# Kernel tuning notes

Hardware: AMD Instinct MI355X
Metric: run time of the kernel (lower is better)

## Reference

```python
import jax, jax.numpy as jnp
import numpy as np

BANDWIDTH = 1.0  # init kwarg: bandwidth; sphere mode -> var_s = gamma = bandwidth
LOG2PI = float(np.log(2.0 * np.pi))


def setup_inputs() -> dict:
    key = jax.random.key(0)
    k1, k2, k3, k4 = jax.random.split(key, 4)
    x = jax.random.normal(k1, (4096, 256), dtype=jnp.float32)
    y = jax.random.normal(k2, (4096, 128), dtype=jnp.float32)
    x_s = jax.random.normal(k3, (8192, 256), dtype=jnp.float32)
    y_s = jax.random.normal(k4, (8192, 128), dtype=jnp.float32)
    return {"x": x, "y": y, "x_s": x_s, "y_s": y_s}


def _sq_dists(a, b):
    # ||a_i - b_j||^2 via GEMM expansion: (batch, num_s)
    a2 = jnp.sum(a * a, axis=-1)[:, None]
    b2 = jnp.sum(b * b, axis=-1)[None, :]
    return a2 + b2 - 2.0 * jnp.einsum("bd,sd->bs", a, b)


def reference(x, y, x_s, y_s):
    x_dim = x.shape[-1]
    y_dim = y.shape[-1]
    var_s = BANDWIDTH
    gamma = BANDWIDTH
    logA_x = x_dim * (LOG2PI + jnp.log(jnp.float32(var_s)))
    logA_y = y_dim * (LOG2PI + jnp.log(jnp.float32(gamma)))

    sdx = _sq_dists(x, x_s) / var_s  # (batch, num_s)
    sdy = _sq_dists(y, y_s) / gamma  # (batch, num_s)

    E_log_pxy = jax.nn.logsumexp(-0.5 * (logA_x + logA_y + sdx + sdy), axis=-1)
    E_log_px = jax.nn.logsumexp(-0.5 * (logA_x + sdx), axis=-1)
    E_log_py = jax.nn.logsumexp(-0.5 * (logA_y + sdy), axis=-1)
    return jnp.mean(E_log_pxy - E_log_px - E_log_py)
```

## Files before the change

### kernel.cpp

```cpp
#include <hip/hip_runtime.h>
#include <hip/hip_bf16.h>
#include <stdint.h>

#define B_N 4096
#define S_N 8192
#define KX  256
#define KY  128
#define BM  128
#define BN  128

#define INV_LN2 1.4426950408889634f
#define LN2_F   0.6931471805599453f

typedef __bf16 bf16x8 __attribute__((ext_vector_type(8)));
typedef float  f32x4  __attribute__((ext_vector_type(4)));

__device__ __forceinline__ float exp2g(float x) { return __builtin_amdgcn_exp2f(x); }
__device__ __forceinline__ float log2g(float x) { return __builtin_amdgcn_logf(x); }

#define OFF_XH   ((size_t)0)
#define OFF_YH   ((size_t)2097152)
#define OFF_SXH  ((size_t)3145728)
#define OFF_SYH  ((size_t)7340032)
#define OFF_NX   ((size_t)9437184)
#define OFF_NY   (OFF_NX + 16384)
#define OFF_NSX  (OFF_NY + 16384)
#define OFF_NSY  (OFF_NSX + 32768)
#define OFF_PART (OFF_NSY + 32768)
#define OFF_BSUM (OFF_PART + (size_t)3*64*4096*2*4)

__device__ __forceinline__ void gl2lds16(const void* g, void* l) {
  typedef const __attribute__((address_space(1))) unsigned int* gp_t;
  typedef __attribute__((address_space(3))) unsigned int* lp_t;
  __builtin_amdgcn_global_load_lds((gp_t)g, (lp_t)l, 16, 0, 0);
}

__device__ __forceinline__ unsigned short f2bf(float f) {
  unsigned u = __builtin_bit_cast(unsigned, f);
  return (unsigned short)((u + 0x7fffu + ((u >> 16) & 1u)) >> 16);
}

__global__ __launch_bounds__(256) void conv_all(const float* __restrict__ x,
                                                const float* __restrict__ y,
                                                const float* __restrict__ xs,
                                                const float* __restrict__ ys,
                                                char* __restrict__ ws) {
  int b    = blockIdx.x;
  int wave = threadIdx.x >> 6;
  int lane = threadIdx.x & 63;
  const float* src; unsigned short* hi; float* nrm;
  int K, row; float scale;
  if (b < 1024) {
    src = x;  hi = (unsigned short*)(ws + OFF_XH);
    nrm = (float*)(ws + OFF_NX); K = 256; row = b * 4 + wave; scale = INV_LN2;
  } else if (b < 2048) {
    src = y;  hi = (unsigned short*)(ws + OFF_YH);
    nrm = (float*)(ws + OFF_NY); K = 128; row = (b - 1024) * 4 + wave; scale = INV_LN2;
  } else if (b < 4096) {
    src = xs; hi = (unsigned short*)(ws + OFF_SXH);
    nrm = (float*)(ws + OFF_NSX); K = 256; row = (b - 2048) * 4 + wave; scale = 1.0f;
  } else {
    src = ys; hi = (unsigned short*)(ws + OFF_SYH);
    nrm = (float*)(ws + OFF_NSY); K = 128; row = (b - 4096) * 4 + wave; scale = 1.0f;
  }
  float acc = 0.f;
  if (K == 256) {
    float4 v = ((const float4*)(src + (size_t)row * 256))[lane];
    float vv[4] = {v.x, v.y, v.z, v.w};
    ushort4 h4;
    unsigned short* hp = (unsigned short*)&h4;
    #pragma unroll
    for (int k = 0; k < 4; ++k) {
      acc = fmaf(vv[k], vv[k], acc);
      hp[k] = f2bf(vv[k] * scale);
    }
    ((ushort4*)(hi + (size_t)row * 256))[lane] = h4;
  } else {
    float2 v = ((const float2*)(src + (size_t)row * 128))[lane];
    float vv[2] = {v.x, v.y};
    ushort2 h2;
    unsigned short* hp = (unsigned short*)&h2;
    #pragma unroll
    for (int k = 0; k < 2; ++k) {
      acc = fmaf(vv[k], vv[k], acc);
      hp[k] = f2bf(vv[k] * scale);
    }
    ((ushort2*)(hi + (size_t)row * 128))[lane] = h2;
  }
  #pragma unroll
  for (int o = 32; o > 0; o >>= 1) acc += __shfl_down(acc, o);
  if (lane == 0) nrm[row] = acc * (-0.5f * INV_LN2);
}

__global__ __launch_bounds__(512, 4) void mie_main(const char* __restrict__ ws,
                                                   float* __restrict__ part) {
  __shared__ __align__(16) char smem[65536];

  const int tid  = threadIdx.x;
  const int lane = tid & 63;
  const int wave = tid >> 6;
  const int c    = lane & 15;
  const int q    = lane >> 4;
  const int wm   = wave >> 1;
  const int wn   = wave & 1;

  const int b     = blockIdx.x;
  const int xcd   = b & 7;
  const int w     = b >> 3;
  const int bm_t  = w & 31;
  const int sn_t  = xcd * 8 + (w >> 5);
  const int bm0   = bm_t * BM;
  const int sn0   = sn_t * BN;

  const char* xh  = ws + OFF_XH;
  const char* yh  = ws + OFF_YH;
  const char* sxh = ws + OFF_SXH;
  const char* syh = ws + OFF_SYH;
  const float* nx  = (const float*)(ws + OFF_NX);
  const float* ny  = (const float*)(ws + OFF_NY);
  const float* nsx = (const float*)(ws + OFF_NSX);
  const float* nsy = (const float*)(ws + OFF_NSY);

  auto stage = [&](int kc, char* base) {
    const char *ah, *bh; int rb, k0b;
    if (kc < 8) { ah = xh; bh = sxh; rb = 512; k0b = kc * 64; }
    else        { ah = yh; bh = syh; rb = 256; k0b = (kc - 8) * 64; }
    int l  = wave * 64 + lane;
    int r  = l >> 2;
    int sl = l & 3;
    int g  = sl ^ ((r >> 1) & 3);
    size_t kofs = (size_t)k0b + (size_t)g * 16;
    size_t goA  = (size_t)(bm0 + r) * rb + kofs;
    size_t goB  = (size_t)(sn0 + r) * rb + kofs;
    char* dst = base + wave * 1024;
    gl2lds16(ah + goA, dst);
    gl2lds16(bh + goB, dst + 8192);
  };

  const int slot = (q ^ ((c >> 1) & 3)) * 16;
  int aoff[2], boff[4];
  #pragma unroll
  for (int i = 0; i < 2; ++i) aoff[i] = (wm * 32 + i * 16 + c) * 64 + slot;
  #pragma unroll
  for (int j = 0; j < 4; ++j) boff[j] = (wn * 64 + j * 16 + c) * 64 + slot;

  f32x4 accx[2][4], accy[2][4];
  #pragma unroll
  for (int i = 0; i < 2; ++i)
    #pragma unroll
    for (int j = 0; j < 4; ++j) {
      accx[i][j] = (f32x4){0.f,0.f,0.f,0.f};
      accy[i][j] = (f32x4){0.f,0.f,0.f,0.f};
    }

  stage(0, smem);
  stage(1, smem + 16384);
  __syncthreads();

  #pragma unroll
  for (int p = 0; p < 6; ++p) {
    if (p < 5) {
      char* nb = smem + ((p + 1) & 1) * 32768;
      stage(2 * p + 2, nb);
      stage(2 * p + 3, nb + 16384);
    }
    const char* bufb = smem + (p & 1) * 32768;
    #pragma unroll
    for (int h = 0; h < 2; ++h) {
      int kc = 2 * p + h;
      const char* base = bufb + h * 16384;
      bf16x8 Ah[2], Bh[4];
      #pragma unroll
      for (int i = 0; i < 2; ++i) Ah[i] = *(const bf16x8*)(base + aoff[i]);
      #pragma unroll
      for (int j = 0; j < 4; ++j) Bh[j] = *(const bf16x8*)(base + 8192 + boff[j]);
      if (kc < 8) {
        #pragma unroll
        for (int i = 0; i < 2; ++i)
          #pragma unroll
          for (int j = 0; j < 4; ++j)
            accx[i][j] = __builtin_amdgcn_mfma_f32_16x16x32_bf16(Ah[i], Bh[j], accx[i][j], 0, 0, 0);
      } else {
        #pragma unroll
        for (int i = 0; i < 2; ++i)
          #pragma unroll
          for (int j = 0; j < 4; ++j)
            accy[i][j] = __builtin_amdgcn_mfma_f32_16x16x32_bf16(Ah[i], Bh[j], accy[i][j], 0, 0, 0);
      }
    }
    __syncthreads();
  }

  float hxv[2][4], hyv[2][4];
  #pragma unroll
  for (int i = 0; i < 2; ++i)
    #pragma unroll
    for (int r = 0; r < 4; ++r) {
      int rr = bm0 + wm * 32 + i * 16 + q * 4 + r;
      hxv[i][r] = nx[rr];
      hyv[i][r] = ny[rr];
    }
  float hsxv[4], hsyv[4];
  #pragma unroll
  for (int j = 0; j < 4; ++j) {
    int cc = sn0 + wn * 64 + j * 16 + c;
    hsxv[j] = nsx[cc];
    hsyv[j] = nsy[cc];
  }

  float2* xch = (float2*)smem;
  #pragma unroll
  for (int i = 0; i < 2; ++i) {
    #pragma unroll
    for (int r = 0; r < 4; ++r) {
      float vx[4], vy[4];
      #pragma unroll
      for (int j = 0; j < 4; ++j) {
        vx[j] = accx[i][j][r] + hxv[i][r] + hsxv[j];
        vy[j] = accy[i][j][r] + hyv[i][r] + hsyv[j];
      }
      int rl = wm * 32 + i * 16 + q * 4 + r;
      #pragma unroll
      for (int st = 0; st < 3; ++st) {
        float v0 = (st == 0) ? vx[0] + vy[0] : (st == 1 ? vx[0] : vy[0]);
        float v1 = (st == 0) ? vx[1] + vy[1] : (st == 1 ? vx[1] : vy[1]);
        float v2 = (st == 0) ? vx[2] + vy[2] : (st == 1 ? vx[2] : vy[2]);
        float v3 = (st == 0) ? vx[3] + vy[3] : (st == 1 ? vx[3] : vy[3]);
        float m = fmaxf(fmaxf(v0, v1), fmaxf(v2, v3));
        #pragma unroll
        for (int msk = 1; msk < 16; msk <<= 1) m = fmaxf(m, __shfl_xor(m, msk));
        float s = exp2g(v0 - m) + exp2g(v1 - m) + exp2g(v2 - m) + exp2g(v3 - m);
        #pragma unroll
        for (int msk = 1; msk < 16; msk <<= 1) s += __shfl_xor(s, msk);
        if (c == 0) xch[(st * 128 + rl) * 2 + wn] = (float2){m, s};
      }
    }
  }
  __syncthreads();

  if (tid < 384) {
    int st = tid >> 7;
    int rl = tid & 127;
    float2 a = xch[(st * 128 + rl) * 2 + 0];
    float2 bb = xch[(st * 128 + rl) * 2 + 1];
    float m = fmaxf(a.x, bb.x);
    float s = a.y * exp2g(a.x - m) + bb.y * exp2g(bb.x - m);
    size_t idx = ((size_t)st * 64 + sn_t) * B_N + (bm0 + rl);
    ((float2*)part)[idx] = (float2){m, s};
  }
}

__global__ __launch_bounds__(256) void fin1(const float* __restrict__ part,
                                            float* __restrict__ bsum) {
  __shared__ float red[4];
  int tid = threadIdx.x;
  int sub = tid & 7;
  int row = blockIdx.x * 32 + (tid >> 3);
  float v[3];
  #pragma unroll
  for (int j = 0; j < 3; ++j) {
    float m = -__builtin_inff(), s = 0.f;
    #pragma unroll
    for (int pp = 0; pp < 8; ++pp) {
      int p = sub * 8 + pp;
      float2 a = ((const float2*)part)[((size_t)j * 64 + p) * B_N + row];
      float nm = fmaxf(m, a.x);
      s = s * exp2g(m - nm) + a.y * exp2g(a.x - nm);
      m = nm;
    }
    #pragma unroll
    for (int msk = 1; msk < 8; msk <<= 1) {
      float om = __shfl_xor(m, msk);
      float os = __shfl_xor(s, msk);
      float nm = fmaxf(m, om);
      s = s * exp2g(m - nm) + os * exp2g(om - nm);
      m = nm;
    }
    v[j] = m + log2g(s);
  }
  float local = (sub == 0) ? (v[0] - v[1] - v[2]) : 0.f;
  #pragma unroll
  for (int o = 32; o > 0; o >>= 1) local += __shfl_down(local, o);
  int wv = tid >> 6, lane = tid & 63;
  if (lane == 0) red[wv] = local;
  __syncthreads();
  if (tid == 0) bsum[blockIdx.x] = red[0] + red[1] + red[2] + red[3];
}

__global__ void fin2(const float* __restrict__ bsum, float* __restrict__ out) {
  int t = threadIdx.x;
  float a = bsum[t] + bsum[t + 64];
  #pragma unroll
  for (int o = 32; o > 0; o >>= 1) a += __shfl_down(a, o);
  if (t == 0) out[0] = a * (LN2_F / (float)B_N);
}

extern "C" void kernel_launch(void* const* d_in, const int* in_sizes, int n_in,
                              void* d_out, int out_size, void* d_ws, size_t ws_size,
                              hipStream_t stream) {
  (void)in_sizes; (void)n_in; (void)out_size; (void)ws_size;
  const float* x  = (const float*)d_in[0];
  const float* y  = (const float*)d_in[1];
  const float* xs = (const float*)d_in[2];
  const float* ys = (const float*)d_in[3];
  char* ws = (char*)d_ws;

  conv_all<<<6144, 256, 0, stream>>>(x, y, xs, ys, ws);
  mie_main<<<2048, 512, 0, stream>>>(ws, (float*)(ws + OFF_PART));
  fin1<<<128, 256, 0, stream>>>((const float*)(ws + OFF_PART), (float*)(ws + OFF_BSUM));
  fin2<<<1, 64, 0, stream>>>((const float*)(ws + OFF_BSUM), (float*)d_out);
}
```

Baseline: 144.7 us.

## Fuse final logsumexp reductions into main kernel via atomic last-block scheme

The two finalize kernels are removed. Their work now runs inside the main kernel: the last 64 blocks to arrive, tracked with an atomic ticket counter, spin until every block has published its partials, then do the per-row merge. The very last of those blocks does the final sum. This saves two kernel launches and their inter-kernel gaps, at the cost of spin-waiting blocks that hold CU slots, plus counter resets done in conv_all.

```diff
diff --git a/kernel.cpp b/kernel.cpp
--- a/kernel.cpp
+++ b/kernel.cpp
@@ -4,10 +4,10 @@
 
 #define B_N 4096
 #define S_N 8192
-#define KX  256
-#define KY  128
 #define BM  128
 #define BN  128
+#define NBLK 2048
+#define NFIN 64
 
 #define INV_LN2 1.4426950408889634f
 #define LN2_F   0.6931471805599453f
@@ -28,6 +28,7 @@
 #define OFF_NSY  (OFF_NSX + 32768)
 #define OFF_PART (OFF_NSY + 32768)
 #define OFF_BSUM (OFF_PART + (size_t)3*64*4096*2*4)
+#define OFF_CTR  (OFF_BSUM + 256)
 
 __device__ __forceinline__ void gl2lds16(const void* g, void* l) {
   typedef const __attribute__((address_space(1))) unsigned int* gp_t;
@@ -45,6 +46,8 @@
                                                 const float* __restrict__ xs,
                                                 const float* __restrict__ ys,
                                                 char* __restrict__ ws) {
+  if (blockIdx.x == 0 && threadIdx.x < 2)
+    ((unsigned*)(ws + OFF_CTR))[threadIdx.x] = 0u;
   int b    = blockIdx.x;
   int wave = threadIdx.x >> 6;
   int lane = threadIdx.x & 63;
@@ -92,8 +95,8 @@
   if (lane == 0) nrm[row] = acc * (-0.5f * INV_LN2);
 }
 
-__global__ __launch_bounds__(512, 4) void mie_main(const char* __restrict__ ws,
-                                                   float* __restrict__ part) {
+__global__ __launch_bounds__(512, 4) void mie_fused(const char* __restrict__ ws,
+                                                    float* __restrict__ out) {
   __shared__ __align__(16) char smem[65536];
 
   const int tid  = threadIdx.x;
@@ -120,6 +123,9 @@
   const float* ny  = (const float*)(ws + OFF_NY);
   const float* nsx = (const float*)(ws + OFF_NSX);
   const float* nsy = (const float*)(ws + OFF_NSY);
+  float* part = (float*)(ws + OFF_PART);
+  float* bsum = (float*)(ws + OFF_BSUM);
+  unsigned* ctr = (unsigned*)(ws + OFF_CTR);
 
   auto stage = [&](int kc, char* base) {
     const char *ah, *bh; int rb, k0b;
@@ -248,51 +254,77 @@
     size_t idx = ((size_t)st * 64 + sn_t) * B_N + (bm0 + rl);
     ((float2*)part)[idx] = (float2){m, s};
   }
-}
-
-__global__ __launch_bounds__(256) void fin1(const float* __restrict__ part,
-                                            float* __restrict__ bsum) {
-  __shared__ float red[4];
-  int tid = threadIdx.x;
-  int sub = tid & 7;
-  int row = blockIdx.x * 32 + (tid >> 3);
-  float v[3];
-  #pragma unroll
-  for (int j = 0; j < 3; ++j) {
-    float m = -__builtin_inff(), s = 0.f;
-    #pragma unroll
-    for (int pp = 0; pp < 8; ++pp) {
-      int p = sub * 8 + pp;
-      float2 a = ((const float2*)part)[((size_t)j * 64 + p) * B_N + row];
-      float nm = fmaxf(m, a.x);
-      s = s * exp2g(m - nm) + a.y * exp2g(a.x - nm);
-      m = nm;
-    }
-    #pragma unroll
-    for (int msk = 1; msk < 8; msk <<= 1) {
-      float om = __shfl_xor(m, msk);
-      float os = __shfl_xor(s, msk);
-      float nm = fmaxf(m, om);
-      s = s * exp2g(m - nm) + os * exp2g(om - nm);
-      m = nm;
-    }
-    v[j] = m + log2g(s);
-  }
-  float local = (sub == 0) ? (v[0] - v[1] - v[2]) : 0.f;
-  #pragma unroll
-  for (int o = 32; o > 0; o >>= 1) local += __shfl_down(local, o);
-  int wv = tid >> 6, lane = tid & 63;
-  if (lane == 0) red[wv] = local;
-  __syncthreads();
-  if (tid == 0) bsum[blockIdx.x] = red[0] + red[1] + red[2] + red[3];
-}
-
-__global__ void fin2(const float* __restrict__ bsum, float* __restrict__ out) {
-  int t = threadIdx.x;
-  float a = bsum[t] + bsum[t + 64];
-  #pragma unroll
-  for (int o = 32; o > 0; o >>= 1) a += __shfl_down(a, o);
-  if (t == 0) out[0] = a * (LN2_F / (float)B_N);
+  __syncthreads();
+
+  unsigned* s_u = (unsigned*)(smem + 8192);
+  if (tid == 0)
+    s_u[0] = __hip_atomic_fetch_add(&ctr[0], 1u, __ATOMIC_ACQ_REL,
+                                    __HIP_MEMORY_SCOPE_AGENT);
+  __syncthreads();
+  unsigned old = s_u[0];
+  if (old < NBLK - NFIN) return;
+
+  if (tid == 0) {
+    while (__hip_atomic_load(&ctr[0], __ATOMIC_ACQUIRE,
+                             __HIP_MEMORY_SCOPE_AGENT) < (unsigned)NBLK)
+      __builtin_amdgcn_s_sleep(2);
+  }
+  __syncthreads();
+
+  int fin_blk = (int)old - (NBLK - NFIN);
+  {
+    float* red = (float*)(smem + 8256);
+    int sub = tid & 7;
+    int row = fin_blk * 64 + (tid >> 3);
+    float v[3];
+    #pragma unroll
+    for (int j = 0; j < 3; ++j) {
+      float m = -__builtin_inff(), s = 0.f;
+      #pragma unroll
+      for (int pp = 0; pp < 8; ++pp) {
+        int p = sub * 8 + pp;
+        float2 a = ((const float2*)part)[((size_t)j * 64 + p) * B_N + row];
+        float nm = fmaxf(m, a.x);
+        s = s * exp2g(m - nm) + a.y * exp2g(a.x - nm);
+        m = nm;
+      }
+      #pragma unroll
+      for (int msk = 1; msk < 8; msk <<= 1) {
+        float om = __shfl_xor(m, msk);
+        float os = __shfl_xor(s, msk);
+        float nm = fmaxf(m, om);
+        s = s * exp2g(m - nm) + os * exp2g(om - nm);
+        m = nm;
+      }
+      v[j] = m + log2g(s);
+    }
+    float local = (sub == 0) ? (v[0] - v[1] - v[2]) : 0.f;
+    #pragma unroll
+    for (int o = 32; o > 0; o >>= 1) local += __shfl_down(local, o);
+    if (lane == 0) red[wave] = local;
+    __syncthreads();
+    if (tid == 0) {
+      float a = 0.f;
+      #pragma unroll
+      for (int u = 0; u < 8; ++u) a += red[u];
+      bsum[fin_blk] = a;
+    }
+  }
+  __syncthreads();
+
+  if (tid == 0)
+    s_u[1] = __hip_atomic_fetch_add(&ctr[1], 1u, __ATOMIC_ACQ_REL,
+                                    __HIP_MEMORY_SCOPE_AGENT);
+  __syncthreads();
+  unsigned o2 = s_u[1];
+  if (o2 == NFIN - 1) {
+    if (tid < 64) {
+      float a = bsum[tid];
+      #pragma unroll
+      for (int o = 32; o > 0; o >>= 1) a += __shfl_down(a, o);
+      if (tid == 0) out[0] = a * (LN2_F / (float)B_N);
+    }
+  }
 }
 
 extern "C" void kernel_launch(void* const* d_in, const int* in_sizes, int n_in,
@@ -306,7 +338,5 @@
   char* ws = (char*)d_ws;
 
   conv_all<<<6144, 256, 0, stream>>>(x, y, xs, ys, ws);
-  mie_main<<<2048, 512, 0, stream>>>(ws, (float*)(ws + OFF_PART));
-  fin1<<<128, 256, 0, stream>>>((const float*)(ws + OFF_PART), (float*)(ws + OFF_BSUM));
-  fin2<<<1, 64, 0, stream>>>((const float*)(ws + OFF_BSUM), (float*)d_out);
-}
+  mie_fused<<<NBLK, 512, 0, stream>>>(ws, (float*)d_out);
+}
```

Result: slower. 197.4 us (+36.5%).
